# Kernel tuning notes

Hardware: AMD Instinct MI355X
Metric: run time of the kernel (lower is better)

## Reference

```python
import jax, jax.numpy as jnp
import numpy as np

GROUP_SIZE = 128
OUT_F, IN_F = 4096, 4096
NUM_GROUPS = OUT_F * IN_F // GROUP_SIZE  # 131072


def setup_inputs() -> dict:
    key = jax.random.key(0)
    k1, k2, k3, k4 = jax.random.split(key, 4)
    x = jax.random.normal(k1, (32, IN_F), dtype=jnp.float32)
    # int4 symmetric quantized weights in [-8, 7]
    q_weight = jax.random.randint(k2, (OUT_F, IN_F), 0, 16, dtype=jnp.int32) - 8
    # per-group positive scales
    weight_scales = jax.random.uniform(k3, (NUM_GROUPS,), dtype=jnp.float32, minval=0.005, maxval=0.02)
    bias = jax.random.normal(k4, (OUT_F,), dtype=jnp.float32)
    return {"x": x, "q_weight": q_weight, "weight_scales": weight_scales, "bias": bias}


def reference(x, q_weight, weight_scales, bias):
    # Group-wise dequant: flatten weight row-major, each contiguous 128-chunk
    # shares one scale (matches GroupWiseQuantizer.dequantize_tensor).
    qf = q_weight.astype(jnp.float32)
    w = (qf.reshape(-1, GROUP_SIZE) * weight_scales[:, None]).reshape(OUT_F, IN_F)
    # F.linear: x @ W^T + b
    return jnp.dot(x, w.T) + bias
```

## Files before the change

### kernel.cpp

```cpp
#include <hip/hip_runtime.h>

typedef __bf16 bf16x8 __attribute__((ext_vector_type(8)));
typedef float f32x4 __attribute__((ext_vector_type(4)));

#define IN_F 4096
#define OUT_F 4096
#define M 32
#define BN 128
#define KC 512
#define KSTEP 64
#define STEPS 8
#define NSPLIT 8
#define NTILE 32

__device__ __forceinline__ void gload16(const void* g, void* l) {
    __builtin_amdgcn_global_load_lds(
        (const __attribute__((address_space(1))) void*)g,
        (__attribute__((address_space(3))) void*)l, 16, 0, 0);
}

template <int N>
__device__ __forceinline__ void wait_vmcnt() {
    asm volatile("s_waitcnt vmcnt(%0)" :: "n"(N) : "memory");
}

__launch_bounds__(512, 2)
__global__ void qlin_gemm(const float* __restrict__ x,
                          const int* __restrict__ qw,
                          const float* __restrict__ scales,
                          float* __restrict__ part) {
    __shared__ int    Wb[3][BN][KSTEP];
    __shared__ __bf16 Xs[M][KC];

    const int t    = threadIdx.x;
    const int lane = t & 63;
    const int wv   = t >> 6;
    const int l16  = lane & 15;
    const int g4   = lane >> 4;
    const int xr   = l16 & 7;

    const int nt    = blockIdx.x & (NTILE - 1);
    const int split = blockIdx.x >> 5;
    const int n0    = nt * BN;
    const int k0    = split * KC;

    const int arow = n0 + wv * 16 + l16;
    const f32x4 sc = *reinterpret_cast<const f32x4*>(
        scales + arow * (IN_F / 128) + split * 4);

    f32x4 a0 = {0.f, 0.f, 0.f, 0.f};
    f32x4 a1 = {0.f, 0.f, 0.f, 0.f};

    auto stageW = [&](int buf, int s) {
        const int kk = k0 + s * KSTEP;
#pragma unroll
        for (int i = 0; i < 4; ++i) {
            const int r    = wv * 16 + i * 4 + g4;
            const int slot = l16 ^ (r & 7);
            gload16(qw + (size_t)(n0 + r) * IN_F + kk + slot * 4,
                    &Wb[buf][wv * 16 + i * 4][0]);
        }
    };

    const int xrow = t >> 4;
    const int cb   = t & 15;
    float4 xa[4], xb[4];
#pragma unroll
    for (int i = 0; i < 4; ++i) {
        const int c = cb + i * 16;
        xa[i] = *reinterpret_cast<const float4*>(x + (size_t)xrow * IN_F + k0 + c * 8);
        xb[i] = *reinterpret_cast<const float4*>(x + (size_t)xrow * IN_F + k0 + c * 8 + 4);
    }
    stageW(0, 0);
    stageW(1, 1);
#pragma unroll
    for (int i = 0; i < 4; ++i) {
        const int c = cb + i * 16;
        bf16x8 v;
        v[0] = (__bf16)xa[i].x; v[1] = (__bf16)xa[i].y;
        v[2] = (__bf16)xa[i].z; v[3] = (__bf16)xa[i].w;
        v[4] = (__bf16)xb[i].x; v[5] = (__bf16)xb[i].y;
        v[6] = (__bf16)xb[i].z; v[7] = (__bf16)xb[i].w;
        const int cs = (c & ~7) | ((c & 7) ^ (xrow & 7));
        *reinterpret_cast<bf16x8*>(&Xs[xrow][cs * 8]) = v;
    }
    asm volatile("" :: "v"(sc[0]), "v"(sc[1]), "v"(sc[2]), "v"(sc[3]));
    __syncthreads();

    auto compute = [&](int buf, int s) {
#pragma unroll
        for (int q = 0; q < 2; ++q) {
            const int s0 = q * 8 + g4 * 2;
            const int4 w0 = *reinterpret_cast<const int4*>(
                &Wb[buf][wv * 16 + l16][((s0)     ^ xr) * 4]);
            const int4 w1 = *reinterpret_cast<const int4*>(
                &Wb[buf][wv * 16 + l16][((s0 + 1) ^ xr) * 4]);
            const float fs = sc[(2 * s + q) >> 2];
            bf16x8 af;
            af[0] = (__bf16)((float)w0.x * fs);
            af[1] = (__bf16)((float)w0.y * fs);
            af[2] = (__bf16)((float)w0.z * fs);
            af[3] = (__bf16)((float)w0.w * fs);
            af[4] = (__bf16)((float)w1.x * fs);
            af[5] = (__bf16)((float)w1.y * fs);
            af[6] = (__bf16)((float)w1.z * fs);
            af[7] = (__bf16)((float)w1.w * fs);
            const int xc = (s * 8) | ((q * 4 + g4) ^ xr);
            const bf16x8 b0 = *reinterpret_cast<const bf16x8*>(&Xs[l16][xc * 8]);
            const bf16x8 b1 = *reinterpret_cast<const bf16x8*>(&Xs[16 + l16][xc * 8]);
            a0 = __builtin_amdgcn_mfma_f32_16x16x32_bf16(af, b0, a0, 0, 0, 0);
            a1 = __builtin_amdgcn_mfma_f32_16x16x32_bf16(af, b1, a1, 0, 0, 0);
        }
    };

#pragma unroll
    for (int s = 0; s < STEPS; ++s) {
        asm volatile("s_waitcnt lgkmcnt(0)" ::: "memory");
        if (s + 2 < STEPS) stageW((s + 2) % 3, s + 2);
        if (s < STEPS - 2)       wait_vmcnt<8>();
        else if (s == STEPS - 2) wait_vmcnt<4>();
        else                     wait_vmcnt<0>();
        compute(s % 3, s);
    }

    float* dst = part + (size_t)split * (M * OUT_F);
    const int nb = n0 + wv * 16 + g4 * 4;
    *reinterpret_cast<f32x4*>(dst + (size_t)l16 * OUT_F + nb)        = a0;
    *reinterpret_cast<f32x4*>(dst + (size_t)(16 + l16) * OUT_F + nb) = a1;
}

__global__ __launch_bounds__(256) void qlin_reduce(const float* __restrict__ part,
                                                   const float* __restrict__ bias,
                                                   float* __restrict__ out) {
    const int i = (blockIdx.x * 256 + threadIdx.x) * 4;
    const int n = i & (OUT_F - 1);
    f32x4 s = *reinterpret_cast<const f32x4*>(bias + n);
#pragma unroll
    for (int p = 0; p < NSPLIT; ++p)
        s += *reinterpret_cast<const f32x4*>(part + (size_t)p * (M * OUT_F) + i);
    *reinterpret_cast<f32x4*>(out + i) = s;
}

__launch_bounds__(512, 2)
__global__ void qlin_fallback(const float* __restrict__ x,
                              const int* __restrict__ qw,
                              const float* __restrict__ scales,
                              const float* __restrict__ bias,
                              float* __restrict__ out) {
    __shared__ float red[8][2][16][20];
    const int t = threadIdx.x, lane = t & 63, wv = t >> 6;
    const int l16 = lane & 15, g = lane >> 4;
    const int n0 = blockIdx.x * 16, row = n0 + l16, kw0 = wv * 512;
    const int*   wp  = qw + row * IN_F + kw0 + g * 8;
    const float* xp0 = x + l16 * IN_F + kw0 + g * 8;
    const float* xp1 = x + (16 + l16) * IN_F + kw0 + g * 8;
    const int scbase = row * (IN_F / 128) + (kw0 >> 7);
    f32x4 acc0 = {0.f,0.f,0.f,0.f}, acc1 = {0.f,0.f,0.f,0.f};
#pragma unroll
    for (int s = 0; s < 16; ++s) {
        const int off = s * 32;
        const int4 w0 = *reinterpret_cast<const int4*>(wp + off);
        const int4 w1 = *reinterpret_cast<const int4*>(wp + off + 4);
        const float scv = scales[scbase + (s >> 2)];
        const float4 xa0 = *reinterpret_cast<const float4*>(xp0 + off);
        const float4 xa1 = *reinterpret_cast<const float4*>(xp0 + off + 4);
        const float4 xb0 = *reinterpret_cast<const float4*>(xp1 + off);
        const float4 xb1 = *reinterpret_cast<const float4*>(xp1 + off + 4);
        bf16x8 af, b0, b1;
        af[0]=(__bf16)((float)w0.x*scv); af[1]=(__bf16)((float)w0.y*scv);
        af[2]=(__bf16)((float)w0.z*scv); af[3]=(__bf16)((float)w0.w*scv);
        af[4]=(__bf16)((float)w1.x*scv); af[5]=(__bf16)((float)w1.y*scv);
        af[6]=(__bf16)((float)w1.z*scv); af[7]=(__bf16)((float)w1.w*scv);
        b0[0]=(__bf16)xa0.x; b0[1]=(__bf16)xa0.y; b0[2]=(__bf16)xa0.z; b0[3]=(__bf16)xa0.w;
        b0[4]=(__bf16)xa1.x; b0[5]=(__bf16)xa1.y; b0[6]=(__bf16)xa1.z; b0[7]=(__bf16)xa1.w;
        b1[0]=(__bf16)xb0.x; b1[1]=(__bf16)xb0.y; b1[2]=(__bf16)xb0.z; b1[3]=(__bf16)xb0.w;
        b1[4]=(__bf16)xb1.x; b1[5]=(__bf16)xb1.y; b1[6]=(__bf16)xb1.z; b1[7]=(__bf16)xb1.w;
        acc0 = __builtin_amdgcn_mfma_f32_16x16x32_bf16(af, b0, acc0, 0,0,0);
        acc1 = __builtin_amdgcn_mfma_f32_16x16x32_bf16(af, b1, acc1, 0,0,0);
    }
    *reinterpret_cast<f32x4*>(&red[wv][0][l16][g*4]) = acc0;
    *reinterpret_cast<f32x4*>(&red[wv][1][l16][g*4]) = acc1;
    __syncthreads();
    const int h = t >> 8, ml = (t >> 4) & 15, nl = t & 15;
    float sum = bias[n0 + nl];
#pragma unroll
    for (int w = 0; w < 8; ++w) sum += red[w][h & 1][ml][nl];
    if (t < 512) out[(h * 16 + ml) * OUT_F + n0 + nl] = sum;
}

extern "C" void kernel_launch(void* const* d_in, const int* in_sizes, int n_in,
                              void* d_out, int out_size, void* d_ws, size_t ws_size,
                              hipStream_t stream) {
    const float* x      = (const float*)d_in[0];
    const int*   qw     = (const int*)d_in[1];
    const float* scales = (const float*)d_in[2];
    const float* bias   = (const float*)d_in[3];
    float* out = (float*)d_out;

    const size_t NEED = (size_t)NSPLIT * M * OUT_F * sizeof(float);
    if (ws_size >= NEED) {
        float* part = (float*)d_ws;
        qlin_gemm<<<dim3(NTILE * NSPLIT), dim3(512), 0, stream>>>(x, qw, scales, part);
        qlin_reduce<<<dim3((M * OUT_F) / (256 * 4)), dim3(256), 0, stream>>>(part, bias, out);
    } else {
        qlin_fallback<<<dim3(OUT_F / 16), dim3(512), 0, stream>>>(
            x, qw, scales, bias, out);
    }
}
```

Baseline: 19.85 us.

## Stage weights through registers and store split-K partials in bf16

```diff
diff --git a/kernel.cpp b/kernel.cpp
--- a/kernel.cpp
+++ b/kernel.cpp
@@ -1,6 +1,7 @@
 #include <hip/hip_runtime.h>
 
 typedef __bf16 bf16x8 __attribute__((ext_vector_type(8)));
+typedef __bf16 bf16x4 __attribute__((ext_vector_type(4)));
 typedef float f32x4 __attribute__((ext_vector_type(4)));
 
 #define IN_F 4096
@@ -13,22 +14,11 @@
 #define NSPLIT 8
 #define NTILE 32
 
-__device__ __forceinline__ void gload16(const void* g, void* l) {
-    __builtin_amdgcn_global_load_lds(
-        (const __attribute__((address_space(1))) void*)g,
-        (__attribute__((address_space(3))) void*)l, 16, 0, 0);
-}
-
-template <int N>
-__device__ __forceinline__ void wait_vmcnt() {
-    asm volatile("s_waitcnt vmcnt(%0)" :: "n"(N) : "memory");
-}
-
-__launch_bounds__(512, 2)
+__launch_bounds__(512, 1)
 __global__ void qlin_gemm(const float* __restrict__ x,
                           const int* __restrict__ qw,
                           const float* __restrict__ scales,
-                          float* __restrict__ part) {
+                          __bf16* __restrict__ part) {
     __shared__ int    Wb[3][BN][KSTEP];
     __shared__ __bf16 Xs[M][KC];
 
@@ -51,14 +41,23 @@
     f32x4 a0 = {0.f, 0.f, 0.f, 0.f};
     f32x4 a1 = {0.f, 0.f, 0.f, 0.f};
 
-    auto stageW = [&](int buf, int s) {
-        const int kk = k0 + s * KSTEP;
+    int4 wA[4], wB[4];
+
+    auto issueW = [&](int4* set, int s) {
 #pragma unroll
         for (int i = 0; i < 4; ++i) {
             const int r    = wv * 16 + i * 4 + g4;
             const int slot = l16 ^ (r & 7);
-            gload16(qw + (size_t)(n0 + r) * IN_F + kk + slot * 4,
-                    &Wb[buf][wv * 16 + i * 4][0]);
+            set[i] = *reinterpret_cast<const int4*>(
+                qw + (size_t)(n0 + r) * IN_F + (k0 + s * KSTEP) + slot * 4);
+        }
+    };
+    auto writeW = [&](int buf, const int4* set) {
+#pragma unroll
+        for (int i = 0; i < 4; ++i) {
+            char* dst = reinterpret_cast<char*>(&Wb[buf][wv * 16 + i * 4][0])
+                      + lane * 16;
+            *reinterpret_cast<int4*>(dst) = set[i];
         }
     };
 
@@ -71,8 +70,8 @@
         xa[i] = *reinterpret_cast<const float4*>(x + (size_t)xrow * IN_F + k0 + c * 8);
         xb[i] = *reinterpret_cast<const float4*>(x + (size_t)xrow * IN_F + k0 + c * 8 + 4);
     }
-    stageW(0, 0);
-    stageW(1, 1);
+    issueW(wA, 0);
+    issueW(wB, 1);
 #pragma unroll
     for (int i = 0; i < 4; ++i) {
         const int c = cb + i * 16;
@@ -86,6 +85,9 @@
     }
     asm volatile("" :: "v"(sc[0]), "v"(sc[1]), "v"(sc[2]), "v"(sc[3]));
     __syncthreads();
+
+    writeW(0, wA);  issueW(wA, 2);
+    writeW(1, wB);  issueW(wB, 3);
 
     auto compute = [&](int buf, int s) {
 #pragma unroll
@@ -115,29 +117,37 @@
 
 #pragma unroll
     for (int s = 0; s < STEPS; ++s) {
-        asm volatile("s_waitcnt lgkmcnt(0)" ::: "memory");
-        if (s + 2 < STEPS) stageW((s + 2) % 3, s + 2);
-        if (s < STEPS - 2)       wait_vmcnt<8>();
-        else if (s == STEPS - 2) wait_vmcnt<4>();
-        else                     wait_vmcnt<0>();
         compute(s % 3, s);
-    }
-
-    float* dst = part + (size_t)split * (M * OUT_F);
+        if (s <= 5) {
+            int4* set = (s & 1) ? wB : wA;
+            writeW((s + 2) % 3, set);
+            if (s <= 3) issueW(set, s + 4);
+        }
+    }
+
+    __bf16* dst = part + (size_t)split * (M * OUT_F);
     const int nb = n0 + wv * 16 + g4 * 4;
-    *reinterpret_cast<f32x4*>(dst + (size_t)l16 * OUT_F + nb)        = a0;
-    *reinterpret_cast<f32x4*>(dst + (size_t)(16 + l16) * OUT_F + nb) = a1;
-}
-
-__global__ __launch_bounds__(256) void qlin_reduce(const float* __restrict__ part,
+    bf16x4 p0, p1;
+#pragma unroll
+    for (int j = 0; j < 4; ++j) { p0[j] = (__bf16)a0[j]; p1[j] = (__bf16)a1[j]; }
+    *reinterpret_cast<bf16x4*>(dst + (size_t)l16 * OUT_F + nb)        = p0;
+    *reinterpret_cast<bf16x4*>(dst + (size_t)(16 + l16) * OUT_F + nb) = p1;
+}
+
+__global__ __launch_bounds__(256) void qlin_reduce(const __bf16* __restrict__ part,
                                                    const float* __restrict__ bias,
                                                    float* __restrict__ out) {
     const int i = (blockIdx.x * 256 + threadIdx.x) * 4;
     const int n = i & (OUT_F - 1);
+    const int m = i >> 12;
     f32x4 s = *reinterpret_cast<const f32x4*>(bias + n);
 #pragma unroll
-    for (int p = 0; p < NSPLIT; ++p)
-        s += *reinterpret_cast<const f32x4*>(part + (size_t)p * (M * OUT_F) + i);
+    for (int p = 0; p < NSPLIT; ++p) {
+        const bf16x4 u = *reinterpret_cast<const bf16x4*>(
+            part + ((size_t)p * M + m) * OUT_F + n);
+#pragma unroll
+        for (int j = 0; j < 4; ++j) s[j] += (float)u[j];
+    }
     *reinterpret_cast<f32x4*>(out + i) = s;
 }
 
@@ -197,9 +207,9 @@
     const float* bias   = (const float*)d_in[3];
     float* out = (float*)d_out;
 
-    const size_t NEED = (size_t)NSPLIT * M * OUT_F * sizeof(float);
+    const size_t NEED = (size_t)NSPLIT * M * OUT_F * sizeof(__bf16);
     if (ws_size >= NEED) {
-        float* part = (float*)d_ws;
+        __bf16* part = (__bf16*)d_ws;
         qlin_gemm<<<dim3(NTILE * NSPLIT), dim3(512), 0, stream>>>(x, qw, scales, part);
         qlin_reduce<<<dim3((M * OUT_F) / (256 * 4)), dim3(256), 0, stream>>>(part, bias, out);
     } else {
```

Measured after the change: 34.56 us. 74.2% more time.
